# Kernel optimization log

Measured on AMD Instinct MI355X. Metric: run time of the kernel, lower is better.

The kernel has to match this reference:

```python
import jax, jax.numpy as jnp
import numpy as np

K = 50
THRESHOLD = 0.3
GAMMA = 1.0
TEMPERATURE = 1.0
MIN_SIM = 0.0
MODE = 'mean'


def _l2_normalize(x, eps=1e-12):
    # matches torch F.normalize(p=2, dim=1): x / max(||x||, eps)
    n = jnp.linalg.norm(x, axis=1, keepdims=True)
    return x / jnp.maximum(n, eps)


def setup_inputs() -> dict:
    key = jax.random.key(0)
    k1, k2, k3 = jax.random.split(key, 3)
    query_features = jax.random.normal(k1, (512, 128), dtype=jnp.float32)
    memory_features = jax.random.normal(k2, (500000, 128), dtype=jnp.float32)
    memory_labels = (jax.random.uniform(k3, (500000, 151)) < 0.1).astype(jnp.float32)
    return {
        'query_features': query_features,
        'memory_features': memory_features,
        'memory_labels': memory_labels,
    }


def reference(query_features, memory_features, memory_labels):
    # fit(): memory is stored L2-normalized; _prepare(): queries normalized
    q = _l2_normalize(query_features)          # [B, D]
    m = _l2_normalize(memory_features)         # [N, D]
    sims = q @ m.T                             # [B, N] cosine similarity
    # min_sim == 0.0 -> no clamping branch
    topk_vals, topk_idx = jax.lax.top_k(sims, K)   # [B, K]
    weights = topk_vals ** GAMMA                   # mode == 'mean'
    neighbours = memory_labels[topk_idx]           # [B, K, L] gather
    numerator = jnp.einsum('bk,bkl->bl', weights, neighbours)
    denominator = jnp.sum(weights, axis=1, keepdims=True) + 1e-8
    scores = numerator / denominator               # [B, L]
    preds = (scores >= THRESHOLD).astype(jnp.int32)
    return preds
```

## Files before the change

kernel.cpp:

```cpp
#include <hip/hip_runtime.h>
#include <math.h>

#define NB   512
#define NM   500000
#define NMP  500224
#define NT16 31264
#define DIM  128
#define KSEL 50
#define NL   151
#define THRESH 0.3f

#define T1F  0.2958f
#define SEG  8
#define NSEG 512
#define MAXC (NSEG * SEG)
#define NHALF 62

typedef float  f32x4  __attribute__((ext_vector_type(4)));
typedef __bf16 bf16x8 __attribute__((ext_vector_type(8)));

__device__ __forceinline__ float wave_reduce_sum(float v) {
  #pragma unroll
  for (int off = 32; off > 0; off >>= 1) v += __shfl_xor(v, off, 64);
  return v;
}

__device__ __forceinline__ unsigned bf16bits(float x) {
  return (unsigned)__builtin_bit_cast(unsigned short, (__bf16)x);
}

template<int CTRL, int RMASK>
__device__ __forceinline__ float dppf0(float x) {
  return __builtin_bit_cast(float,
      __builtin_amdgcn_update_dpp(0, __builtin_bit_cast(int, x), CTRL, RMASK, 0xf, true));
}

__device__ __forceinline__ float dpp_sum32(float x) {
  x += dppf0<0x111, 0xf>(x);
  x += dppf0<0x112, 0xf>(x);
  x += dppf0<0x114, 0xf>(x);
  x += dppf0<0x118, 0xf>(x);
  x += dppf0<0x142, 0xa>(x);
  return x;
}

template<int CTRL, int RMASK>
__device__ __forceinline__ void dpp_pmax_step(float& v, int& ix) {
  float v2 = __builtin_bit_cast(float, __builtin_amdgcn_update_dpp(
      __builtin_bit_cast(int, -3e30f), __builtin_bit_cast(int, v), CTRL, RMASK, 0xf, false));
  int i2 = __builtin_amdgcn_update_dpp(0x7fffffff, ix, CTRL, RMASK, 0xf, false);
  if (v2 > v || (v2 == v && i2 < ix)) { v = v2; ix = i2; }
}

__device__ __forceinline__ void dpp_pmax64(float& v, int& ix, float& Wv, int& Wix) {
  dpp_pmax_step<0x111, 0xf>(v, ix);
  dpp_pmax_step<0x112, 0xf>(v, ix);
  dpp_pmax_step<0x114, 0xf>(v, ix);
  dpp_pmax_step<0x118, 0xf>(v, ix);
  dpp_pmax_step<0x142, 0xa>(v, ix);
  dpp_pmax_step<0x143, 0xc>(v, ix);
  Wv  = __builtin_bit_cast(float, __builtin_amdgcn_readlane(__builtin_bit_cast(int, v), 63));
  Wix = __builtin_amdgcn_readlane(ix, 63);
}

__global__ void normalize_q(const float* __restrict__ q, float* __restrict__ qn,
                            __bf16* __restrict__ qbf) {
  int w = threadIdx.x >> 6, lane = threadIdx.x & 63;
  int row = blockIdx.x * 4 + w;
  float2 v = *reinterpret_cast<const float2*>(q + row * DIM + lane * 2);
  float ss = wave_reduce_sum(v.x * v.x + v.y * v.y);
  float n = fmaxf(sqrtf(ss), 1e-12f);
  float a = v.x / n, b = v.y / n;
  *reinterpret_cast<float2*>(qn + row * DIM + lane * 2) = make_float2(a, b);
  reinterpret_cast<unsigned*>(qbf)[row * 64 + lane] = bf16bits(a) | (bf16bits(b) << 16);
}

__global__ __launch_bounds__(512, 4) void sims1(
    const float* __restrict__ mem, const __bf16* __restrict__ qbf,
    int* __restrict__ cntseg, int* __restrict__ cseg)
{
  __shared__ __align__(16) __bf16 mt[2][16 * DIM];
  __shared__ __align__(16) float thr[2][16];
  __shared__ int lcnt[NB];
  __shared__ int lhit[NB * SEG];

  const int t = threadIdx.x;
  const int wv = t >> 6, lane = t & 63;
  const int lq = lane & 15, lk = lane >> 4;
  const int x = blockIdx.x;
  const int q0 = wv * 64;
  const int srow = t >> 5;
  const int scol = t & 31;

  lcnt[t] = 0;

  bf16x8 bq[4][4];
  #pragma unroll
  for (int jq = 0; jq < 4; ++jq)
    #pragma unroll
    for (int kk = 0; kk < 4; ++kk)
      bq[jq][kk] = *reinterpret_cast<const bf16x8*>(
          qbf + (q0 + jq * 16 + lq) * DIM + kk * 32 + lk * 8);

  auto tlid = [&](int k) { int tt = x + k * NSEG; return tt < NT16 ? tt : (NT16 - 1); };

  auto gload = [&](int k, f32x4& r) {
    long row = (long)tlid(k) * 16 + srow;
    r = (row < NM) ? *reinterpret_cast<const f32x4*>(mem + row * DIM + scol * 4)
                   : (f32x4){0.f, 0.f, 0.f, 0.f};
  };

  auto cstore = [&](const f32x4& r, int b) {
    float ss = dpp_sum32(r[0]*r[0] + r[1]*r[1] + r[2]*r[2] + r[3]*r[3]);
    uint2 o;
    o.x = bf16bits(r[0]) | (bf16bits(r[1]) << 16);
    o.y = bf16bits(r[2]) | (bf16bits(r[3]) << 16);
    char* lb = reinterpret_cast<char*>(&mt[b][0]);
    int c16 = scol >> 1;
    *reinterpret_cast<uint2*>(lb + srow * 256 + ((((c16 + srow) & 15)) << 4)
                              + ((scol & 1) << 3)) = o;
    if (scol == 31) thr[b][srow] = T1F * sqrtf(ss);
  };

  auto half = [&](int k, int b, f32x4& rnext) {
    const char* lb = reinterpret_cast<const char*>(&mt[b][0]);
    bf16x8 am[4];
    #pragma unroll
    for (int kk = 0; kk < 4; ++kk)
      am[kk] = *reinterpret_cast<const bf16x8*>(
          lb + lq * 256 + ((((kk << 2) + lk + lq) & 15) << 4));
    f32x4 tv = *reinterpret_cast<const f32x4*>(&thr[b][lk << 2]);

    f32x4 acc[4];
    #pragma unroll
    for (int jq = 0; jq < 4; ++jq) acc[jq] = (f32x4){0.f, 0.f, 0.f, 0.f};
    __builtin_amdgcn_s_setprio(1);
    #pragma unroll
    for (int kk = 0; kk < 4; ++kk)
      #pragma unroll
      for (int jq = 0; jq < 4; ++jq)
        acc[jq] = __builtin_amdgcn_mfma_f32_16x16x32_bf16(am[kk], bq[jq][kk], acc[jq], 0, 0, 0);
    __builtin_amdgcn_s_setprio(0);

    const int row0 = tlid(k) * 16 + lk * 4;
    #pragma unroll
    for (int jq = 0; jq < 4; ++jq) {
      f32x4 a = acc[jq];
      float mx = fmaxf(fmaxf(a[0] - tv[0], a[1] - tv[1]),
                       fmaxf(a[2] - tv[2], a[3] - tv[3]));
      if (mx > 0.f) {
        int qq = q0 + jq * 16 + lq;
        #pragma unroll
        for (int j = 0; j < 4; ++j)
          if (a[j] > tv[j]) {
            int p = atomicAdd(&lcnt[qq], 1);
            if (p < SEG) lhit[qq * SEG + p] = row0 + j;
          }
      }
    }
    cstore(rnext, b ^ 1);
    asm volatile("s_waitcnt lgkmcnt(0)" ::: "memory");
    __builtin_amdgcn_s_barrier();
  };

  f32x4 ra, rb;
  gload(0, ra);
  gload(1, rb);
  cstore(ra, 0);
  __syncthreads();

  #pragma unroll 1
  for (int k = 0; k < NHALF; k += 2) {
    gload(k + 2, ra);
    half(k, 0, rb);
    gload(k + 3, rb);
    half(k + 1, 1, ra);
  }

  __syncthreads();
  #pragma unroll
  for (int i = t; i < NB * SEG; i += 512) {
    int ql = i >> 3, s = i & 7;
    if (s < lcnt[ql]) cseg[(ql * NSEG + x) * SEG + s] = lhit[i];
  }
  if (t < NB) cntseg[t * NSEG + x] = min(lcnt[t], SEG);
}

__global__ __launch_bounds__(256) void select_score(
    const float* __restrict__ mem, const float* __restrict__ qn,
    const float* __restrict__ labels, const int* __restrict__ cntseg,
    const int* __restrict__ cseg, int* __restrict__ out)
{
  __shared__ int   lidx[MAXC];
  __shared__ float sval[MAXC];
  __shared__ int   snc;
  __shared__ float lw[KSEL];
  __shared__ int   li[KSEL];
  __shared__ float s_wsum;

  const int q = blockIdx.x, t = threadIdx.x;
  const int hw = t >> 5, l32 = t & 31;

  if (t == 0) snc = 0;
  __syncthreads();

  for (int i = t; i < NSEG * SEG; i += 256) {
    int x = i >> 3, s = i & 7;
    if (s < cntseg[q * NSEG + x]) {
      int id = cseg[(q * NSEG + x) * SEG + s];
      int p = atomicAdd(&snc, 1);
      lidx[p] = id;
    }
  }
  __syncthreads();
  const int nc = snc;

  f32x4 qv = *reinterpret_cast<const f32x4*>(qn + q * DIM + l32 * 4);
  for (int base = hw * 4; base < nc; base += 32) {
    int id[4]; f32x4 mv[4];
    #pragma unroll
    for (int s = 0; s < 4; ++s)
      if (base + s < nc) id[s] = lidx[base + s];
    #pragma unroll
    for (int s = 0; s < 4; ++s)
      if (base + s < nc)
        mv[s] = *reinterpret_cast<const f32x4*>(mem + (size_t)id[s] * DIM + l32 * 4);
    #pragma unroll
    for (int s = 0; s < 4; ++s)
      if (base + s < nc) {
        float d = mv[s][0]*qv[0] + mv[s][1]*qv[1] + mv[s][2]*qv[2] + mv[s][3]*qv[3];
        float e = mv[s][0]*mv[s][0] + mv[s][1]*mv[s][1] + mv[s][2]*mv[s][2] + mv[s][3]*mv[s][3];
        d = dpp_sum32(d);
        e = dpp_sum32(e);
        if (l32 == 31) sval[base + s] = d / fmaxf(sqrtf(e), 1e-12f);
      }
  }
  __syncthreads();

  if (t < 64) {
    const int ksel = nc < KSEL ? nc : KSEL;
    float wsum = 0.f;
    if (nc <= 512) {
      float rv[8]; int rix[8];
      #pragma unroll
      for (int s = 0; s < 8; ++s) {
        int i = t + s * 64;
        bool ok = i < nc;
        rv[s]  = ok ? sval[i] : -3e30f;
        rix[s] = ok ? lidx[i] : 0x7fffffff;
      }
      for (int it = 0; it < ksel; ++it) {
        float bv = rv[0]; int bix = rix[0];
        #pragma unroll
        for (int s = 1; s < 8; ++s)
          if (rv[s] > bv || (rv[s] == bv && rix[s] < bix)) { bv = rv[s]; bix = rix[s]; }
        float Wv; int Wix;
        dpp_pmax64(bv, bix, Wv, Wix);
        if (t == 0) { lw[it] = Wv; li[it] = Wix; }
        wsum += Wv;
        #pragma unroll
        for (int s = 0; s < 8; ++s)
          if (rix[s] == Wix) rv[s] = -3e30f;
      }
    } else {
      for (int it = 0; it < ksel; ++it) {
        float bv = -3e30f; int bix = 0x7fffffff;
        for (int i = t; i < nc; i += 64) {
          float v = sval[i]; int ix = lidx[i];
          if (v > bv || (v == bv && ix < bix)) { bv = v; bix = ix; }
        }
        float Wv; int Wix;
        dpp_pmax64(bv, bix, Wv, Wix);
        if (t == 0) { lw[it] = Wv; li[it] = Wix; }
        wsum += Wv;
        for (int i = t; i < nc; i += 64)
          if (lidx[i] == Wix) sval[i] = -3e30f;
      }
    }
    if (t == 0) s_wsum = wsum;
  }
  __syncthreads();

  if (t < NL) {
    const int ksel = nc < KSEL ? nc : KSEL;
    float num = 0.f;
    for (int j0 = 0; j0 < ksel; j0 += 4) {
      float lv[4];
      #pragma unroll
      for (int s = 0; s < 4; ++s)
        lv[s] = (j0 + s < ksel) ? labels[(size_t)li[j0 + s] * NL + t] : 0.f;
      #pragma unroll
      for (int s = 0; s < 4; ++s)
        if (j0 + s < ksel) num += lw[j0 + s] * lv[s];
    }
    float sc = num / (s_wsum + 1e-8f);
    out[q * NL + t] = (sc >= THRESH) ? 1 : 0;
  }
}

extern "C" void kernel_launch(void* const* d_in, const int* in_sizes, int n_in,
                              void* d_out, int out_size, void* d_ws, size_t ws_size,
                              hipStream_t stream)
{
  const float* qf = (const float*)d_in[0];
  const float* mf = (const float*)d_in[1];
  const float* ml = (const float*)d_in[2];
  int* out = (int*)d_out;

  char* ws = (char*)d_ws;
  size_t o = 0;
  float*  qn     = (float*)(ws + o);  o += (size_t)NB * DIM * 4;
  __bf16* qbf    = (__bf16*)(ws + o); o += (size_t)NB * DIM * 2;
  int*    cntseg = (int*)(ws + o);    o += (size_t)NB * NSEG * 4;
  int*    cseg   = (int*)(ws + o);

  normalize_q<<<NB / 4, 256, 0, stream>>>(qf, qn, qbf);
  sims1<<<NSEG, 512, 0, stream>>>(mf, qbf, cntseg, cseg);
  select_score<<<NB, 256, 0, stream>>>(mf, qn, ml, cntseg, cseg, out);
}
```

Baseline: 145.4 us.

## Stream memory tiles via async global_load_lds into 4-stage fp32 LDS ring

Replaces register-staged loads plus a bf16 conversion-store into a double-buffered LDS tile with direct global-to-LDS async loads into a 4-deep ring of fp32 tiles. The loads are pre-swizzled so LDS reads avoid bank conflicts. Each wave now converts to bf16 and computes row norms itself after reading from LDS. The loop also drops the padded tile count and uses a per-block exact trip count. This aims to hide HBM latency with deeper prefetch and remove VGPR staging, at the cost of twice the LDS per tile and redundant per-wave conversion and norm work.

New measurement: 230.7 us. 58.6% more time.

```diff
diff --git a/kernel.cpp b/kernel.cpp
--- a/kernel.cpp
+++ b/kernel.cpp
@@ -3,8 +3,7 @@
 
 #define NB   512
 #define NM   500000
-#define NMP  500224
-#define NT16 31264
+#define NT   31250
 #define DIM  128
 #define KSEL 50
 #define NL   151
@@ -14,7 +13,6 @@
 #define SEG  8
 #define NSEG 512
 #define MAXC (NSEG * SEG)
-#define NHALF 62
 
 typedef float  f32x4  __attribute__((ext_vector_type(4)));
 typedef __bf16 bf16x8 __attribute__((ext_vector_type(8)));
@@ -61,6 +59,13 @@
   dpp_pmax_step<0x143, 0xc>(v, ix);
   Wv  = __builtin_bit_cast(float, __builtin_amdgcn_readlane(__builtin_bit_cast(int, v), 63));
   Wix = __builtin_amdgcn_readlane(ix, 63);
+}
+
+__device__ __forceinline__ bf16x8 cvt8(f32x4 a, f32x4 b) {
+  bf16x8 r;
+  r[0] = (__bf16)a[0]; r[1] = (__bf16)a[1]; r[2] = (__bf16)a[2]; r[3] = (__bf16)a[3];
+  r[4] = (__bf16)b[0]; r[5] = (__bf16)b[1]; r[6] = (__bf16)b[2]; r[7] = (__bf16)b[3];
+  return r;
 }
 
 __global__ void normalize_q(const float* __restrict__ q, float* __restrict__ qn,
@@ -79,8 +84,7 @@
     const float* __restrict__ mem, const __bf16* __restrict__ qbf,
     int* __restrict__ cntseg, int* __restrict__ cseg)
 {
-  __shared__ __align__(16) __bf16 mt[2][16 * DIM];
-  __shared__ __align__(16) float thr[2][16];
+  __shared__ __align__(16) float mt[4][16 * DIM];
   __shared__ int lcnt[NB];
   __shared__ int lhit[NB * SEG];
 
@@ -89,8 +93,6 @@
   const int lq = lane & 15, lk = lane >> 4;
   const int x = blockIdx.x;
   const int q0 = wv * 64;
-  const int srow = t >> 5;
-  const int scol = t & 31;
 
   lcnt[t] = 0;
 
@@ -102,47 +104,87 @@
       bq[jq][kk] = *reinterpret_cast<const bf16x8*>(
           qbf + (q0 + jq * 16 + lq) * DIM + kk * 32 + lk * 8);
 
-  auto tlid = [&](int k) { int tt = x + k * NSEG; return tt < NT16 ? tt : (NT16 - 1); };
-
-  auto gload = [&](int k, f32x4& r) {
-    long row = (long)tlid(k) * 16 + srow;
-    r = (row < NM) ? *reinterpret_cast<const f32x4*>(mem + row * DIM + scol * 4)
-                   : (f32x4){0.f, 0.f, 0.f, 0.f};
+  const int nt = (NT - x + NSEG - 1) / NSEG;
+  const int sr = t >> 5;
+  const int scs = ((t & 31) - sr) & 31;
+  const char* gmem = reinterpret_cast<const char*>(mem);
+
+  auto stage = [&](int k, int b) {
+    int kc = k < nt ? k : nt - 1;
+    const char* gb = gmem + (size_t)(x + kc * NSEG) * 8192;
+    __builtin_amdgcn_global_load_lds(
+        (const __attribute__((address_space(1))) unsigned int*)(gb + sr * 512 + scs * 16),
+        (__attribute__((address_space(3))) unsigned int*)(
+            reinterpret_cast<char*>(&mt[b][0]) + t * 16),
+        16, 0, 0);
   };
 
-  auto cstore = [&](const f32x4& r, int b) {
-    float ss = dpp_sum32(r[0]*r[0] + r[1]*r[1] + r[2]*r[2] + r[3]*r[3]);
-    uint2 o;
-    o.x = bf16bits(r[0]) | (bf16bits(r[1]) << 16);
-    o.y = bf16bits(r[2]) | (bf16bits(r[3]) << 16);
-    char* lb = reinterpret_cast<char*>(&mt[b][0]);
-    int c16 = scol >> 1;
-    *reinterpret_cast<uint2*>(lb + srow * 256 + ((((c16 + srow) & 15)) << 4)
-                              + ((scol & 1) << 3)) = o;
-    if (scol == 31) thr[b][srow] = T1F * sqrtf(ss);
-  };
-
-  auto half = [&](int k, int b, f32x4& rnext) {
-    const char* lb = reinterpret_cast<const char*>(&mt[b][0]);
-    bf16x8 am[4];
-    #pragma unroll
-    for (int kk = 0; kk < 4; ++kk)
-      am[kk] = *reinterpret_cast<const bf16x8*>(
-          lb + lq * 256 + ((((kk << 2) + lk + lq) & 15) << 4));
-    f32x4 tv = *reinterpret_cast<const f32x4*>(&thr[b][lk << 2]);
+  asm volatile("s_waitcnt vmcnt(0)" ::: "memory");
+  stage(0, 0); stage(1, 1); stage(2, 2);
+  asm volatile("s_waitcnt lgkmcnt(0)" ::: "memory");
+  __builtin_amdgcn_s_barrier();
+
+  #pragma unroll 1
+  for (int k = 0; k < nt; ++k) {
+    asm volatile("s_waitcnt vmcnt(2)" ::: "memory");
+    __builtin_amdgcn_s_barrier();
+    __builtin_amdgcn_sched_barrier(0);
+
+    stage(k + 3, (k + 3) & 3);
+
+    const float* lb = &mt[k & 3][0];
+    const int rbase = lq * 128;
+
+    f32x4 f0 = *reinterpret_cast<const f32x4*>(lb + rbase + (((lk * 2 + 0) + lq) & 31) * 4);
+    f32x4 f1 = *reinterpret_cast<const f32x4*>(lb + rbase + (((lk * 2 + 1) + lq) & 31) * 4);
+    f32x4 f2 = *reinterpret_cast<const f32x4*>(lb + rbase + (((8 + lk * 2 + 0) + lq) & 31) * 4);
+    f32x4 f3 = *reinterpret_cast<const f32x4*>(lb + rbase + (((8 + lk * 2 + 1) + lq) & 31) * 4);
+    float ssp = f0[0]*f0[0] + f0[1]*f0[1] + f0[2]*f0[2] + f0[3]*f0[3]
+              + f1[0]*f1[0] + f1[1]*f1[1] + f1[2]*f1[2] + f1[3]*f1[3]
+              + f2[0]*f2[0] + f2[1]*f2[1] + f2[2]*f2[2] + f2[3]*f2[3]
+              + f3[0]*f3[0] + f3[1]*f3[1] + f3[2]*f3[2] + f3[3]*f3[3];
+    bf16x8 a0 = cvt8(f0, f1), a1 = cvt8(f2, f3);
 
     f32x4 acc[4];
     #pragma unroll
     for (int jq = 0; jq < 4; ++jq) acc[jq] = (f32x4){0.f, 0.f, 0.f, 0.f};
+
     __builtin_amdgcn_s_setprio(1);
     #pragma unroll
-    for (int kk = 0; kk < 4; ++kk)
-      #pragma unroll
-      for (int jq = 0; jq < 4; ++jq)
-        acc[jq] = __builtin_amdgcn_mfma_f32_16x16x32_bf16(am[kk], bq[jq][kk], acc[jq], 0, 0, 0);
+    for (int jq = 0; jq < 4; ++jq)
+      acc[jq] = __builtin_amdgcn_mfma_f32_16x16x32_bf16(a0, bq[jq][0], acc[jq], 0, 0, 0);
+    #pragma unroll
+    for (int jq = 0; jq < 4; ++jq)
+      acc[jq] = __builtin_amdgcn_mfma_f32_16x16x32_bf16(a1, bq[jq][1], acc[jq], 0, 0, 0);
     __builtin_amdgcn_s_setprio(0);
 
-    const int row0 = tlid(k) * 16 + lk * 4;
+    f0 = *reinterpret_cast<const f32x4*>(lb + rbase + (((16 + lk * 2 + 0) + lq) & 31) * 4);
+    f1 = *reinterpret_cast<const f32x4*>(lb + rbase + (((16 + lk * 2 + 1) + lq) & 31) * 4);
+    f2 = *reinterpret_cast<const f32x4*>(lb + rbase + (((24 + lk * 2 + 0) + lq) & 31) * 4);
+    f3 = *reinterpret_cast<const f32x4*>(lb + rbase + (((24 + lk * 2 + 1) + lq) & 31) * 4);
+    ssp += f0[0]*f0[0] + f0[1]*f0[1] + f0[2]*f0[2] + f0[3]*f0[3]
+         + f1[0]*f1[0] + f1[1]*f1[1] + f1[2]*f1[2] + f1[3]*f1[3]
+         + f2[0]*f2[0] + f2[1]*f2[1] + f2[2]*f2[2] + f2[3]*f2[3]
+         + f3[0]*f3[0] + f3[1]*f3[1] + f3[2]*f3[2] + f3[3]*f3[3];
+    bf16x8 a2 = cvt8(f0, f1), a3 = cvt8(f2, f3);
+
+    ssp += __shfl_xor(ssp, 16);
+    ssp += __shfl_xor(ssp, 32);
+    float nrm = T1F * sqrtf(ssp);
+    float tv[4];
+    #pragma unroll
+    for (int j = 0; j < 4; ++j) tv[j] = __shfl(nrm, lk * 4 + j);
+
+    __builtin_amdgcn_s_setprio(1);
+    #pragma unroll
+    for (int jq = 0; jq < 4; ++jq)
+      acc[jq] = __builtin_amdgcn_mfma_f32_16x16x32_bf16(a2, bq[jq][2], acc[jq], 0, 0, 0);
+    #pragma unroll
+    for (int jq = 0; jq < 4; ++jq)
+      acc[jq] = __builtin_amdgcn_mfma_f32_16x16x32_bf16(a3, bq[jq][3], acc[jq], 0, 0, 0);
+    __builtin_amdgcn_s_setprio(0);
+
+    const int row0 = (x + k * NSEG) * 16 + lk * 4;
     #pragma unroll
     for (int jq = 0; jq < 4; ++jq) {
       f32x4 a = acc[jq];
@@ -158,23 +200,6 @@
           }
       }
     }
-    cstore(rnext, b ^ 1);
-    asm volatile("s_waitcnt lgkmcnt(0)" ::: "memory");
-    __builtin_amdgcn_s_barrier();
-  };
-
-  f32x4 ra, rb;
-  gload(0, ra);
-  gload(1, rb);
-  cstore(ra, 0);
-  __syncthreads();
-
-  #pragma unroll 1
-  for (int k = 0; k < NHALF; k += 2) {
-    gload(k + 2, ra);
-    half(k, 0, rb);
-    gload(k + 3, rb);
-    half(k + 1, 1, ra);
   }
 
   __syncthreads();
```

## Deepen sims1 pipeline to four LDS buffers with one barrier per tile pair

Applied to the files above, without the earlier changes.

Replaces the two-buffer, barrier-per-tile loop in the similarity kernel with a four-buffer ring. Two tiles are computed per barrier while the next two tiles are staged into LDS and two more are prefetched from global memory. This halves the number of workgroup barriers and gives global loads more time to land. In exchange it raises shared memory use and register pressure for the extra in-flight loads. Each block now walks 64 tiles instead of 62, so the extra tiles are zero-filled, out-of-range work.

After: 213.3 us. +46.7%, slower.

```diff
diff --git a/kernel.cpp b/kernel.cpp
--- a/kernel.cpp
+++ b/kernel.cpp
@@ -14,7 +14,6 @@
 #define SEG  8
 #define NSEG 512
 #define MAXC (NSEG * SEG)
-#define NHALF 62
 
 typedef float  f32x4  __attribute__((ext_vector_type(4)));
 typedef __bf16 bf16x8 __attribute__((ext_vector_type(8)));
@@ -79,8 +78,8 @@
     const float* __restrict__ mem, const __bf16* __restrict__ qbf,
     int* __restrict__ cntseg, int* __restrict__ cseg)
 {
-  __shared__ __align__(16) __bf16 mt[2][16 * DIM];
-  __shared__ __align__(16) float thr[2][16];
+  __shared__ __align__(16) __bf16 mt[4][16 * DIM];
+  __shared__ __align__(16) float thr[4][16];
   __shared__ int lcnt[NB];
   __shared__ int lhit[NB * SEG];
 
@@ -122,7 +121,7 @@
     if (scol == 31) thr[b][srow] = T1F * sqrtf(ss);
   };
 
-  auto half = [&](int k, int b, f32x4& rnext) {
+  auto comp = [&](int k, int b) {
     const char* lb = reinterpret_cast<const char*>(&mt[b][0]);
     bf16x8 am[4];
     #pragma unroll
@@ -142,7 +141,7 @@
         acc[jq] = __builtin_amdgcn_mfma_f32_16x16x32_bf16(am[kk], bq[jq][kk], acc[jq], 0, 0, 0);
     __builtin_amdgcn_s_setprio(0);
 
-    const int row0 = tlid(k) * 16 + lk * 4;
+    const int row0 = (x + k * NSEG) * 16 + lk * 4;
     #pragma unroll
     for (int jq = 0; jq < 4; ++jq) {
       f32x4 a = acc[jq];
@@ -158,23 +157,30 @@
           }
       }
     }
-    cstore(rnext, b ^ 1);
+  };
+
+  f32x4 g0, g1, s0, s1;
+  { f32x4 r; gload(0, r); cstore(r, 0); gload(1, r); cstore(r, 1); }
+  gload(2, s0); gload(3, s1);
+  __syncthreads();
+
+  #pragma unroll 1
+  for (int j = 0; j < 64; j += 4) {
+    gload(j + 4, g0); gload(j + 5, g1);
+    comp(j + 0, (j + 0) & 3);
+    comp(j + 1, (j + 1) & 3);
+    cstore(s0, (j + 2) & 3);
+    cstore(s1, (j + 3) & 3);
     asm volatile("s_waitcnt lgkmcnt(0)" ::: "memory");
     __builtin_amdgcn_s_barrier();
-  };
-
-  f32x4 ra, rb;
-  gload(0, ra);
-  gload(1, rb);
-  cstore(ra, 0);
-  __syncthreads();
-
-  #pragma unroll 1
-  for (int k = 0; k < NHALF; k += 2) {
-    gload(k + 2, ra);
-    half(k, 0, rb);
-    gload(k + 3, rb);
-    half(k + 1, 1, ra);
+
+    gload(j + 6, s0); gload(j + 7, s1);
+    comp(j + 2, (j + 2) & 3);
+    comp(j + 3, (j + 3) & 3);
+    cstore(g0, (j + 4) & 3);
+    cstore(g1, (j + 5) & 3);
+    asm volatile("s_waitcnt lgkmcnt(0)" ::: "memory");
+    __builtin_amdgcn_s_barrier();
   }
 
   __syncthreads();
```

## Compact candidate lists via global atomics instead of per-segment slots

Applied to the files above, without the earlier changes.

The first-pass kernel now appends each query's candidates to a compact per-query list, using a global atomic counter capped at 1024 entries. Previously it wrote a fixed 8-slot array per segment plus a count array. The select kernel then reads the dense list directly, with no scan over 4096 slots and shared atomics, and runs with 512 threads instead of 256. This removes the sparse gather and the large segment array, at the cost of global atomics, an extra memset launch, and silently dropping candidates if a query exceeds the cap.

Measured after the change: 138.3 us (median of 2 runs). -4.9%, faster.

```diff
diff --git a/kernel.cpp b/kernel.cpp
--- a/kernel.cpp
+++ b/kernel.cpp
@@ -13,7 +13,7 @@
 #define T1F  0.2958f
 #define SEG  8
 #define NSEG 512
-#define MAXC (NSEG * SEG)
+#define CAPQ 1024
 #define NHALF 62
 
 typedef float  f32x4  __attribute__((ext_vector_type(4)));
@@ -77,7 +77,7 @@
 
 __global__ __launch_bounds__(512, 4) void sims1(
     const float* __restrict__ mem, const __bf16* __restrict__ qbf,
-    int* __restrict__ cntseg, int* __restrict__ cseg)
+    int* __restrict__ gcnt, int* __restrict__ gidx)
 {
   __shared__ __align__(16) __bf16 mt[2][16 * DIM];
   __shared__ __align__(16) float thr[2][16];
@@ -178,45 +178,37 @@
   }
 
   __syncthreads();
-  #pragma unroll
-  for (int i = t; i < NB * SEG; i += 512) {
-    int ql = i >> 3, s = i & 7;
-    if (s < lcnt[ql]) cseg[(ql * NSEG + x) * SEG + s] = lhit[i];
-  }
-  if (t < NB) cntseg[t * NSEG + x] = min(lcnt[t], SEG);
-}
-
-__global__ __launch_bounds__(256) void select_score(
+  if (t < NB) {
+    int c = lcnt[t]; if (c > SEG) c = SEG;
+    if (c > 0) {
+      int base = atomicAdd(&gcnt[t], c);
+      #pragma unroll 1
+      for (int s = 0; s < c; ++s)
+        if (base + s < CAPQ) gidx[t * CAPQ + base + s] = lhit[t * SEG + s];
+    }
+  }
+}
+
+__global__ __launch_bounds__(512) void select_score(
     const float* __restrict__ mem, const float* __restrict__ qn,
-    const float* __restrict__ labels, const int* __restrict__ cntseg,
-    const int* __restrict__ cseg, int* __restrict__ out)
+    const float* __restrict__ labels, const int* __restrict__ gcnt,
+    const int* __restrict__ gidx, int* __restrict__ out)
 {
-  __shared__ int   lidx[MAXC];
-  __shared__ float sval[MAXC];
-  __shared__ int   snc;
+  __shared__ int   lidx[CAPQ];
+  __shared__ float sval[CAPQ];
   __shared__ float lw[KSEL];
   __shared__ int   li[KSEL];
   __shared__ float s_wsum;
 
   const int q = blockIdx.x, t = threadIdx.x;
   const int hw = t >> 5, l32 = t & 31;
-
-  if (t == 0) snc = 0;
-  __syncthreads();
-
-  for (int i = t; i < NSEG * SEG; i += 256) {
-    int x = i >> 3, s = i & 7;
-    if (s < cntseg[q * NSEG + x]) {
-      int id = cseg[(q * NSEG + x) * SEG + s];
-      int p = atomicAdd(&snc, 1);
-      lidx[p] = id;
-    }
-  }
-  __syncthreads();
-  const int nc = snc;
+  const int nc = min(gcnt[q], CAPQ);
+
+  for (int i = t; i < nc; i += 512) lidx[i] = gidx[q * CAPQ + i];
+  __syncthreads();
 
   f32x4 qv = *reinterpret_cast<const f32x4*>(qn + q * DIM + l32 * 4);
-  for (int base = hw * 4; base < nc; base += 32) {
+  for (int base = hw * 4; base < nc; base += 64) {
     int id[4]; f32x4 mv[4];
     #pragma unroll
     for (int s = 0; s < 4; ++s)
@@ -309,12 +301,13 @@
 
   char* ws = (char*)d_ws;
   size_t o = 0;
-  float*  qn     = (float*)(ws + o);  o += (size_t)NB * DIM * 4;
-  __bf16* qbf    = (__bf16*)(ws + o); o += (size_t)NB * DIM * 2;
-  int*    cntseg = (int*)(ws + o);    o += (size_t)NB * NSEG * 4;
-  int*    cseg   = (int*)(ws + o);
-
+  float*  qn   = (float*)(ws + o);  o += (size_t)NB * DIM * 4;
+  __bf16* qbf  = (__bf16*)(ws + o); o += (size_t)NB * DIM * 2;
+  int*    gcnt = (int*)(ws + o);    o += (size_t)NB * 4;
+  int*    gidx = (int*)(ws + o);
+
+  hipMemsetAsync(gcnt, 0, NB * sizeof(int), stream);
   normalize_q<<<NB / 4, 256, 0, stream>>>(qf, qn, qbf);
-  sims1<<<NSEG, 512, 0, stream>>>(mf, qbf, cntseg, cseg);
-  select_score<<<NB, 256, 0, stream>>>(mf, qn, ml, cntseg, cseg, out);
-}
+  sims1<<<NSEG, 512, 0, stream>>>(mf, qbf, gcnt, gidx);
+  select_score<<<NB, 512, 0, stream>>>(mf, qn, ml, gcnt, gidx, out);
+}
```
